# Kernel optimization log

Measured on AMD Instinct MI355X. Metric: run time of the kernel, lower is better.

## Reference

```python
import jax, jax.numpy as jnp
import numpy as np

B, L, D, H, V = 4, 128, 128, 8, 32000
N_ITER = 4
DAMP_H = DAMP_Z = DAMP_X = 0.0
STEP_H = STEP_Z = STEP_X = 1.0
REG_H = REG_Z = REG_X = 1.0
BLOCK_MSG = False
NEG = 1e9


def _norm(t):
    # norm='softmax'
    return jax.nn.softmax(t, axis=-1)


def setup_inputs() -> dict:
    key = jax.random.key(0)
    k1, k2, k3, k4 = jax.random.split(key, 4)
    x = jax.random.normal(k1, (B, L, D), dtype=jnp.float32)
    mask = jnp.ones((B, L), dtype=jnp.int32)
    m_mask = jax.random.randint(k2, (B, L), 0, 2).astype(jnp.int32)
    embed_matrix = jax.random.normal(k3, (V, D), dtype=jnp.float32)
    ternary = jax.random.normal(k4, (2, D, D, H), dtype=jnp.float32)  # dists='' -> 2 groups
    return {"x": x, "mask": mask, "embed_matrix": embed_matrix, "m_mask": m_mask, "ternary": ternary}


def _forward(x, mask, embed_matrix, m_mask, ternary):
    dt = x.dtype
    mask1d = mask != 0                                   # [B,L] True = real token
    valid2d = mask1d[:, :, None] & mask1d[:, None, :]    # [B,L,L]
    inv2d = ~valid2d[:, None, :, :]                      # broadcast over heads
    keep = mask1d[..., None].astype(dt)                  # [B,L,1]
    mm = m_mask.astype(dt)[..., None]                    # [B,L,1]

    # distance mask: dists='' -> [triu(1); tril(-1)] -> [2,L,L]
    dm = jnp.triu(jnp.ones((L, L), dt), 1)
    distmask = jnp.stack([dm, dm.T], axis=0)

    eye = jnp.eye(L, dtype=dt)

    unary = x
    q_x = jnp.ones((B, L, V), dt)
    # initialize_Z=True: masked positions start from expected embedding
    pre = _norm(q_x) @ embed_matrix                      # [B,L,D]
    q_z = unary * (1.0 - mm) + pre * mm
    q_z = q_z * keep

    q_h = jnp.ones((B, H, L, L), dt) - eye * NEG
    q_h = jnp.where(inv2d, -NEG, q_h)

    cache_qh, cache_qz, cache_qx = q_h, q_z, q_x
    # async_update=True: normalize Z before first H update
    q_z = _norm(q_z) * keep

    for _ in range(N_ITER):
        # ---- H update: F[z,c,i,j] = sum_{k,a,b} q_z[z,i,a] q_z[z,j,b] T[k,a,b,c] dist[k,i,j]
        t1 = jnp.einsum('zia,kabc->zkibc', q_z, ternary)            # [B,2,L,D,H]
        F = jnp.einsum('zkibc,zjb,kij->zcij', t1, q_z, distmask)    # [B,H,L,L]
        q_h = cache_qh * DAMP_H + F * (1.0 - DAMP_H) / REG_H
        q_h = cache_qh * (1.0 - STEP_H) + q_h * STEP_H
        cache_qh = q_h
        q_h = q_h - eye * NEG
        q_h = jnp.where(inv2d, -NEG, q_h)
        q_hn = _norm(q_h)                                           # [B,H,L,L]

        # ---- Z update: first-order messages from ternary factors
        m = q_hn[:, None] * distmask[None, :, None]                 # [B,2,H,L,L]
        s1 = jnp.einsum('zkcij,zjb->zkibc', m, q_z)                 # to Z_i (head slot)
        G = jnp.einsum('zkibc,kabc->zia', s1, ternary)
        if not BLOCK_MSG:
            s2 = jnp.einsum('zkcij,zia->zkjac', m, q_z)             # to Z_j (dep slot)
            G = G + jnp.einsum('zkjac,kabc->zjb', s2, ternary)

        # unary: X message replaces word unary at <MASK> positions
        unary_eff = unary * (1.0 - mm) + (_norm(q_x) @ embed_matrix) * mm
        q_z_new = cache_qz * DAMP_Z + (unary_eff + G) * (1.0 - DAMP_Z) / REG_Z
        q_z_new = cache_qz * (1.0 - STEP_Z) + q_z_new * STEP_Z
        cache_qz = q_z_new
        q_z = _norm(q_z_new) * keep

        # ---- X update: message from Z through embedding factor
        msg_x = jnp.einsum('zia,va->ziv', q_z, embed_matrix)        # [B,L,V]
        q_x_new = cache_qx * DAMP_X + msg_x * (1.0 - DAMP_X) / REG_X
        q_x_new = cache_qx * (1.0 - STEP_X) + q_x_new * STEP_X
        cache_qx = q_x_new
        q_x = q_x_new

    # output_prob=False -> unnormalized scores
    return q_x


def reference(x, mask, embed_matrix, m_mask, ternary):
    return _forward(x, mask, embed_matrix, m_mask, ternary)
```

## Files before the change

kernel.cpp:

```cpp
#include <hip/hip_runtime.h>
#include <math.h>

#define L_ 128
#define D_ 128
#define H_ 8
#define V_ 32000
#define NEGC 1e9f

typedef short short8 __attribute__((ext_vector_type(8)));
typedef float f32x4 __attribute__((ext_vector_type(4)));
typedef unsigned short ushort8v __attribute__((ext_vector_type(8)));

__device__ __forceinline__ unsigned short f2bf(float x) {
    unsigned int u = __float_as_uint(x);
    unsigned int r = (u + 0x7fff + ((u >> 16) & 1)) >> 16;
    return (unsigned short)r;
}


__global__ __launch_bounds__(256) void colsum_k(const float* __restrict__ E, float* __restrict__ meansum) {
    int t = threadIdx.x;
    int d = t & 127, h = t >> 7;
    int v0 = blockIdx.x * 256;
    float s = 0.f;
    for (int p = 0; p < 128; ++p)
        s += E[(v0 + h + 2 * p) * 128 + d];
    __shared__ float red[256];
    red[t] = s;
    __syncthreads();
    if (h == 0) atomicAdd(&meansum[d], red[d] + red[128 + d]);
}

__global__ __launch_bounds__(256) void frag_k(const float* __restrict__ E,
                                              unsigned short* __restrict__ Ebf,
                                              unsigned short* __restrict__ Etf) {
    __shared__ unsigned short tile[32][136];
    int t = threadIdx.x;
    int b = blockIdx.x;
    int v0 = b * 32;
#pragma unroll
    for (int i = 0; i < 4; ++i) {
        int idx = i * 256 + t;
        int v = idx >> 5;
        int d4 = (idx & 31) * 4;
        float4 val = *(const float4*)&E[(size_t)(v0 + v) * 128 + d4];
        tile[v][d4 + 0] = f2bf(val.x);
        tile[v][d4 + 1] = f2bf(val.y);
        tile[v][d4 + 2] = f2bf(val.z);
        tile[v][d4 + 3] = f2bf(val.w);
    }
    __syncthreads();
    {
        int fi = t >> 5;
        int l0 = (t & 31) * 2;
        int vtl = fi >> 2, s = fi & 3;
        size_t base = ((size_t)(b * 2 + vtl) * 4 + s) * 512;
#pragma unroll
        for (int li = 0; li < 2; ++li) {
            int l = l0 + li;
            int nl = l & 15, hf = l >> 4;
            ushort8v o;
#pragma unroll
            for (int j = 0; j < 8; ++j) o[j] = tile[vtl * 16 + nl][s * 32 + hf * 8 + j];
            *(ushort8v*)&Ebf[base + l * 8] = o;
        }
    }
    {
        int ct = t >> 5;
        int l0 = (t & 31) * 2;
        size_t base = ((size_t)b * 8 + ct) * 512;
#pragma unroll
        for (int li = 0; li < 2; ++li) {
            int l = l0 + li;
            int nl = l & 15, hf = l >> 4;
            ushort8v o;
#pragma unroll
            for (int j = 0; j < 8; ++j) o[j] = tile[hf * 8 + j][ct * 16 + nl];
            *(ushort8v*)&Etf[base + l * 8] = o;
        }
    }
}

__global__ __launch_bounds__(256) void transT_k(const float* __restrict__ T, float* __restrict__ Tt) {
    for (int q = 0; q < 4; ++q) {
        int id = blockIdx.x * 1024 + q * 256 + threadIdx.x;
        int k = id >> 17;
        int rem = id & 131071;
        int a = rem >> 10;
        int bc = rem & 1023;
        int b = bc >> 3, c = bc & 7;
        Tt[k * 131072 + b * 1024 + a * 8 + c] = T[id];
    }
}

__global__ __launch_bounds__(512) void compact_k(const int* __restrict__ m_mask,
                                                 int* __restrict__ rowidx, int* __restrict__ nactb) {
    int t = threadIdx.x;
    bool act = m_mask[t] != 0;
    unsigned long long b = __ballot(act);
    int w = t >> 6, lane = t & 63;
    __shared__ int wc[8];
    if (lane == 0) wc[w] = __popcll(b);
    __syncthreads();
    int base = 0;
    for (int i = 0; i < w; ++i) base += wc[i];
    if (act) rowidx[base + __popcll(b & ((1ull << lane) - 1))] = t;
    if (t == 0) {
        int tot = 0;
        for (int i = 0; i < 8; ++i) tot += wc[i];
        nactb[0] = tot;
    }
}

__global__ __launch_bounds__(64) void init_k(const float* __restrict__ x, const int* __restrict__ mask,
                                             const int* __restrict__ m_mask, const float* __restrict__ meansum,
                                             float* __restrict__ ue, float* __restrict__ qz,
                                             unsigned short* __restrict__ qzb) {
    int row = blockIdx.x, t = threadIdx.x;
    float keepv = mask[row] ? 1.f : 0.f;
    bool mm = m_mask[row] != 0;
    float pre0 = meansum[t] * (1.f / 32000.f);
    float pre1 = meansum[t + 64] * (1.f / 32000.f);
    float u0 = mm ? pre0 : x[row * 128 + t];
    float u1 = mm ? pre1 : x[row * 128 + t + 64];
    ue[row * 128 + t] = u0;
    ue[row * 128 + t + 64] = u1;
    float sv0 = u0 * keepv, sv1 = u1 * keepv;
    float m = fmaxf(sv0, sv1);
    for (int off = 32; off; off >>= 1) m = fmaxf(m, __shfl_xor(m, off));
    float e0 = __expf(sv0 - m), e1 = __expf(sv1 - m);
    float s = e0 + e1;
    for (int off = 32; off; off >>= 1) s += __shfl_xor(s, off);
    float inv = keepv / s;
    float q0 = e0 * inv, q1 = e1 * inv;
    qz[row * 128 + t] = q0;
    qz[row * 128 + t + 64] = q1;
    qzb[row * 128 + t] = f2bf(q0);
    qzb[row * 128 + t + 64] = f2bf(q1);
}


__global__ __launch_bounds__(256) void pxe_k(const unsigned short* __restrict__ qzb,
                                             const unsigned short* __restrict__ Ebf,
                                             const unsigned short* __restrict__ Etf,
                                             const int* __restrict__ rowidx, const int* __restrict__ nactb,
                                             float* __restrict__ partial, float* __restrict__ partial_rs) {
    int nact = nactb[0];
    int bid = blockIdx.x;
    int xcd = bid & 7, idx = bid >> 3;
    int g = xcd + 8 * (idx >> 5);
    int bx = idx & 31;
    int r0 = bx * 16;
    if (g >= 50 || r0 >= nact) return;
    int t = threadIdx.x;
    int w = t >> 6, lane = t & 63;
    int nloc = lane & 15, half = lane >> 4;
    __shared__ __align__(16) unsigned short Pl[4][2][16 * 36];
    __shared__ float slab[4][16 * 130];
    __shared__ float rsW[4][16];
    int rA = r0 + nloc;
    bool actA = rA < nact;
    int rowA = actA ? rowidx[rA] : 0;
    short8 zero8 = (short8){0, 0, 0, 0, 0, 0, 0, 0};
    short8 afr[4];
#pragma unroll
    for (int s = 0; s < 4; ++s) {
        short8 v = *(const short8*)&qzb[rowA * 128 + s * 32 + half * 8];
        afr[s] = actA ? v : zero8;
    }
    const int kc0 = g * 20 + w * 5;
    short8 ebb[2][8];
#pragma unroll
    for (int f = 0; f < 8; ++f)
        ebb[0][f] = *(const short8*)&Ebf[((size_t)(kc0 * 8 + f)) * 512 + lane * 8];
    f32x4 acc2[8];
#pragma unroll
    for (int ct = 0; ct < 8; ++ct) acc2[ct] = (f32x4){0.f, 0.f, 0.f, 0.f};
    float rsl = 0.f;
#pragma unroll
    for (int step = 0; step < 5; ++step) {
        const int p = step & 1;
        const int kc = kc0 + step;
        short8 et[8];
#pragma unroll
        for (int f = 0; f < 8; ++f)
            et[f] = *(const short8*)&Etf[((size_t)(kc * 8 + f)) * 512 + lane * 8];
        if (step < 4) {
#pragma unroll
            for (int f = 0; f < 8; ++f)
                ebb[p ^ 1][f] = *(const short8*)&Ebf[((size_t)((kc + 1) * 8 + f)) * 512 + lane * 8];
        }
        f32x4 p0 = (f32x4){0.f, 0.f, 0.f, 0.f};
        f32x4 p1 = (f32x4){0.f, 0.f, 0.f, 0.f};
#pragma unroll
        for (int s = 0; s < 4; ++s) {
            p0 = __builtin_amdgcn_mfma_f32_16x16x32_bf16(ebb[p][s], afr[s], p0, 0, 0, 0);
            p1 = __builtin_amdgcn_mfma_f32_16x16x32_bf16(ebb[p][4 + s], afr[s], p1, 0, 0, 0);
        }
        unsigned short* pw = &Pl[w][p][0];
        {
            float e0 = __expf(p0[0]), e1 = __expf(p0[1]), e2 = __expf(p0[2]), e3 = __expf(p0[3]);
            rsl += (e0 + e1) + (e2 + e3);
            uint2 pk = {(unsigned)f2bf(e0) | ((unsigned)f2bf(e1) << 16),
                        (unsigned)f2bf(e2) | ((unsigned)f2bf(e3) << 16)};
            *(uint2*)&pw[nloc * 36 + half * 4] = pk;
        }
        {
            float e0 = __expf(p1[0]), e1 = __expf(p1[1]), e2 = __expf(p1[2]), e3 = __expf(p1[3]);
            rsl += (e0 + e1) + (e2 + e3);
            uint2 pk = {(unsigned)f2bf(e0) | ((unsigned)f2bf(e1) << 16),
                        (unsigned)f2bf(e2) | ((unsigned)f2bf(e3) << 16)};
            *(uint2*)&pw[nloc * 36 + 16 + half * 4] = pk;
        }
        short8 a2 = *(const short8*)&pw[nloc * 36 + half * 8];
#pragma unroll
        for (int ct = 0; ct < 8; ++ct)
            acc2[ct] = __builtin_amdgcn_mfma_f32_16x16x32_bf16(a2, et[ct], acc2[ct], 0, 0, 0);
    }
    rsl += __shfl_xor(rsl, 16);
    rsl += __shfl_xor(rsl, 32);
    if (lane < 16) rsW[w][nloc] = rsl;
#pragma unroll
    for (int ct = 0; ct < 8; ++ct)
#pragma unroll
        for (int reg = 0; reg < 4; ++reg)
            slab[w][(half * 4 + reg) * 130 + ct * 16 + nloc] = acc2[ct][reg];
    __syncthreads();
    float* pb = partial + (size_t)g * 65536;
    for (int i = t; i < 2048; i += 256) {
        int row = i >> 7, col = i & 127;
        int rr = r0 + row;
        if (rr < nact)
            pb[rr * 128 + col] = slab[0][row * 130 + col] + slab[1][row * 130 + col]
                               + slab[2][row * 130 + col] + slab[3][row * 130 + col];
    }
    if (t < 16) {
        int rr = r0 + t;
        if (rr < nact)
            partial_rs[g * 512 + rr] = rsW[0][t] + rsW[1][t] + rsW[2][t] + rsW[3][t];
    }
}

__global__ __launch_bounds__(256) void reduce_k(const float* __restrict__ partial,
                                                const float* __restrict__ partial_rs,
                                                const int* __restrict__ rowidx, const int* __restrict__ nactb,
                                                float* __restrict__ exbuf, float* __restrict__ rowsum) {
    int nact = nactb[0];
    int idx = blockIdx.x * 256 + threadIdx.x;
    int rr = idx >> 7, col = idx & 127;
    if (rr >= nact) return;
    float s = 0.f;
#pragma unroll 10
    for (int g = 0; g < 50; ++g)
        s += partial[(size_t)g * 65536 + rr * 128 + col];
    int row = rowidx[rr];
    exbuf[row * 128 + col] = s;
    if (col == 0) {
        float ts = 0.f;
#pragma unroll 10
        for (int g = 0; g < 50; ++g) ts += partial_rs[g * 512 + rr];
        rowsum[row] = ts;
    }
}

__global__ __launch_bounds__(256) void uwgemm_k(const float* __restrict__ qz, const float* __restrict__ T,
                                                const float* __restrict__ Tt, float* __restrict__ U2,
                                                unsigned short* __restrict__ Ut, unsigned short* __restrict__ Wt) {
    int t = threadIdx.x;
    int by = blockIdx.y;
    int uw = by >> 3, z = (by >> 1) & 3, k = by & 1;
    int bx = blockIdx.x;
    int m0 = (bx >> 2) * 16, n = (bx & 3) * 256 + t;
    const float* A = qz + z * 16384;
    const float* Bm = (uw ? Tt : T) + k * 131072;
    __shared__ float aL[2048];
    for (int idx = t; idx < 2048; idx += 256)
        aL[idx] = A[(m0 + (idx >> 7)) * 128 + (idx & 127)];
    __syncthreads();
    float acc[16];
#pragma unroll
    for (int m = 0; m < 16; ++m) acc[m] = 0.f;
    for (int kq = 0; kq < 32; ++kq) {
        float b0 = Bm[(kq * 4 + 0) * 1024 + n];
        float b1 = Bm[(kq * 4 + 1) * 1024 + n];
        float b2 = Bm[(kq * 4 + 2) * 1024 + n];
        float b3 = Bm[(kq * 4 + 3) * 1024 + n];
#pragma unroll
        for (int m = 0; m < 16; ++m) {
            const float4 aq = *(const float4*)&aL[m * 128 + kq * 4];
            acc[m] += aq.x * b0 + aq.y * b1 + aq.z * b2 + aq.w * b3;
        }
    }
    if (uw == 0) {
        float* Cm = U2 + (z * 2 + k) * 131072;
#pragma unroll
        for (int m = 0; m < 16; ++m)
            Cm[(m0 + m) * 1024 + n] = acc[m];
    }
    int bb = n >> 3, cc = n & 7;
    ushort8v p0, p1;
#pragma unroll
    for (int m = 0; m < 8; ++m) { p0[m] = f2bf(acc[m]); p1[m] = f2bf(acc[8 + m]); }
    unsigned short* To = (uw ? Wt : Ut) + ((size_t)(z * 2 + k) * 128 + bb) * 1024 + cc * 128 + m0;
    *(ushort8v*)&To[0] = p0;
    *(ushort8v*)&To[8] = p1;
}

__global__ __launch_bounds__(256) void qhnF_k(const float* __restrict__ qz, const float* __restrict__ U2,
                                              const int* __restrict__ mask,
                                              unsigned short* __restrict__ A0b, unsigned short* __restrict__ A1b,
                                              unsigned short* __restrict__ A0Tb, unsigned short* __restrict__ A1Tb) {
    int bx = blockIdx.x;
    int z = bx >> 6, c = (bx >> 3) & 7, iq = bx & 7;
    int i0 = iq * 16;
    int t = threadIdx.x;
    int tj = t & 15, ti = t >> 4;
    int i = i0 + ti;
    __shared__ float As[2][16][36];
    __shared__ float Bs[128][36];
    __shared__ int maskL[128];
    if (t < 128) maskL[t] = mask[z * 128 + t];
    float acc0[8], acc1[8];
#pragma unroll
    for (int jj = 0; jj < 8; ++jj) { acc0[jj] = 0.f; acc1[jj] = 0.f; }
    const float* U2z = U2 + (size_t)z * 262144;
    const float* qzz = qz + z * 16384;
    for (int kb = 0; kb < 4; ++kb) {
        int b0 = kb * 32;
        __syncthreads();
        for (int e = t; e < 1024; e += 256) {
            int k = e >> 9, r = e & 511, ii = r >> 5, b = r & 31;
            As[k][ii][b] = U2z[k * 131072 + (i0 + ii) * 1024 + (b0 + b) * 8 + c];
        }
        for (int f = t; f < 1024; f += 256) {
            int j = f >> 3, b4 = f & 7;
            int slot = b4 ^ ((j >> 3) & 7);
            *(float4*)&Bs[j][slot * 4] = *(const float4*)&qzz[j * 128 + b0 + b4 * 4];
        }
        __syncthreads();
#pragma unroll
        for (int b4 = 0; b4 < 8; ++b4) {
            float4 a0 = *(const float4*)&As[0][ti][b4 * 4];
            float4 a1 = *(const float4*)&As[1][ti][b4 * 4];
#pragma unroll
            for (int jj = 0; jj < 8; ++jj) {
                int j = tj * 8 + jj;
                int slot = b4 ^ ((j >> 3) & 7);
                float4 bq = *(const float4*)&Bs[j][slot * 4];
                acc0[jj] += a0.x * bq.x;
                acc0[jj] += a0.y * bq.y;
                acc0[jj] += a0.z * bq.z;
                acc0[jj] += a0.w * bq.w;
                acc1[jj] += a1.x * bq.x;
                acc1[jj] += a1.y * bq.y;
                acc1[jj] += a1.z * bq.z;
                acc1[jj] += a1.w * bq.w;
            }
        }
    }
    bool vi = maskL[i] != 0;
    float fv[8];
#pragma unroll
    for (int jj = 0; jj < 8; ++jj) {
        int j2 = tj * 8 + jj;
        float F = (j2 > i) ? acc0[jj] : acc1[jj];
        if (j2 == i) F -= NEGC;
        if (!vi || maskL[j2] == 0) F = -NEGC;
        fv[jj] = F;
    }
    float mval = fv[0];
#pragma unroll
    for (int jj = 1; jj < 8; ++jj) mval = fmaxf(mval, fv[jj]);
    for (int off = 1; off < 16; off <<= 1) mval = fmaxf(mval, __shfl_xor(mval, off));
    float ssum = 0.f;
#pragma unroll
    for (int jj = 0; jj < 8; ++jj) ssum += __expf(fv[jj] - mval);
    for (int off = 1; off < 16; off <<= 1) ssum += __shfl_xor(ssum, off);
    float inv = 1.f / ssum;
    size_t base = (size_t)(z * 8 + c) * 16384;
    ushort8v v0, v1;
    unsigned short bvv[8];
#pragma unroll
    for (int jj = 0; jj < 8; ++jj) {
        int j2 = tj * 8 + jj;
        float val = __expf(fv[jj] - mval) * inv;
        unsigned short bv = f2bf(val);
        bvv[jj] = bv;
        v0[jj] = (j2 > i) ? bv : (unsigned short)0;
        v1[jj] = (j2 < i) ? bv : (unsigned short)0;
    }
    *(ushort8v*)&A0b[base + i * 128 + tj * 8] = v0;
    *(ushort8v*)&A1b[base + i * 128 + tj * 8] = v1;
#pragma unroll
    for (int jj = 0; jj < 8; ++jj) {
        int j2 = tj * 8 + jj;
        A0Tb[base + j2 * 128 + i] = (i < j2) ? bvv[jj] : (unsigned short)0;
        A1Tb[base + j2 * 128 + i] = (i > j2) ? bvv[jj] : (unsigned short)0;
    }
}

__global__ __launch_bounds__(64) void gkern_mfma_k(const unsigned short* __restrict__ A0b,
                                                   const unsigned short* __restrict__ A1b,
                                                   const unsigned short* __restrict__ A0Tb,
                                                   const unsigned short* __restrict__ A1Tb,
                                                   const unsigned short* __restrict__ Ut,
                                                   const unsigned short* __restrict__ Wt,
                                                   float* __restrict__ g1, float* __restrict__ g2) {
    int mode = blockIdx.y;
    int bx = blockIdx.x;
    int z = bx >> 6, it = (bx >> 3) & 7, at = bx & 7;
    int lane = threadIdx.x;
    int nloc = lane & 15, half = lane >> 4;
    int i0 = it * 16, a0 = at * 16;
    const unsigned short* Am0 = (mode ? A0Tb : A0b) + (size_t)z * 131072;
    const unsigned short* Am1 = (mode ? A1Tb : A1b) + (size_t)z * 131072;
    const unsigned short* Bt = mode ? Ut : Wt;
    const unsigned short* B0 = Bt + (size_t)(z * 2 + 0) * 131072 + (size_t)(a0 + nloc) * 1024;
    const unsigned short* B1 = Bt + (size_t)(z * 2 + 1) * 131072 + (size_t)(a0 + nloc) * 1024;
    const unsigned short* Ar0 = Am0 + (size_t)(i0 + nloc) * 128;
    const unsigned short* Ar1 = Am1 + (size_t)(i0 + nloc) * 128;
    f32x4 acc = (f32x4){0.f, 0.f, 0.f, 0.f};
#pragma unroll
    for (int c = 0; c < 8; ++c) {
#pragma unroll
        for (int sb = 0; sb < 4; ++sb) {
            int s0 = sb * 32 + half * 8;
            short8 av0 = *(const short8*)&Ar0[c * 16384 + s0];
            short8 bv0 = *(const short8*)&B0[c * 128 + s0];
            acc = __builtin_amdgcn_mfma_f32_16x16x32_bf16(av0, bv0, acc, 0, 0, 0);
            short8 av1 = *(const short8*)&Ar1[c * 16384 + s0];
            short8 bv1 = *(const short8*)&B1[c * 128 + s0];
            acc = __builtin_amdgcn_mfma_f32_16x16x32_bf16(av1, bv1, acc, 0, 0, 0);
        }
    }
    float* G = mode ? g2 : g1;
#pragma unroll
    for (int reg = 0; reg < 4; ++reg)
        G[(z * 128 + i0 + half * 4 + reg) * 128 + a0 + nloc] = acc[reg];
}

__global__ __launch_bounds__(64) void zupd_k(const float* __restrict__ ue, const float* __restrict__ x,
                                             const int* __restrict__ m_mask,
                                             const float* __restrict__ exbuf, const float* __restrict__ rowsum,
                                             const float* __restrict__ g1, const float* __restrict__ g2,
                                             const int* __restrict__ mask,
                                             float* __restrict__ qz, unsigned short* __restrict__ qzb, int useEx) {
    int row = blockIdx.x, t = threadIdx.x;
    float keepv = mask[row] ? 1.f : 0.f;
    int b = row * 128;
    float u0, u1;
    if (useEx) {
        if (m_mask[row] != 0) {
            float rsv = rowsum[row];
            u0 = exbuf[b + t] / rsv;
            u1 = exbuf[b + t + 64] / rsv;
        } else {
            u0 = x[b + t];
            u1 = x[b + t + 64];
        }
    } else {
        u0 = ue[b + t];
        u1 = ue[b + t + 64];
    }
    float v0 = u0 + g1[b + t] + g2[b + t];
    float v1 = u1 + g1[b + t + 64] + g2[b + t + 64];
    float m = fmaxf(v0, v1);
    for (int off = 32; off; off >>= 1) m = fmaxf(m, __shfl_xor(m, off));
    float e0 = __expf(v0 - m), e1 = __expf(v1 - m);
    float s = e0 + e1;
    for (int off = 32; off; off >>= 1) s += __shfl_xor(s, off);
    float inv = keepv / s;
    float q0 = e0 * inv, q1 = e1 * inv;
    qz[b + t] = q0;
    qz[b + t + 64] = q1;
    qzb[b + t] = f2bf(q0);
    qzb[b + t + 64] = f2bf(q1);
}

__global__ __launch_bounds__(256) void msgx_mfma_k(const unsigned short* __restrict__ qzb,
                                                   const unsigned short* __restrict__ Ebf,
                                                   float* __restrict__ out) {
    int t = threadIdx.x;
    int w = t >> 6, lane = t & 63;
    int nloc = lane & 15, half = lane >> 4;
    int rt0 = blockIdx.x * 64;
    int cb0 = blockIdx.y * 256 + w * 64;
    short8 afr[4][4];
#pragma unroll
    for (int r = 0; r < 4; ++r)
#pragma unroll
        for (int s = 0; s < 4; ++s)
            afr[r][s] = *(const short8*)&qzb[(rt0 + r * 16 + nloc) * 128 + s * 32 + half * 8];
    f32x4 acc[4][4];
#pragma unroll
    for (int r = 0; r < 4; ++r)
#pragma unroll
        for (int ct = 0; ct < 4; ++ct)
            acc[r][ct] = (f32x4){0.f, 0.f, 0.f, 0.f};
#pragma unroll
    for (int ct = 0; ct < 4; ++ct) {
#pragma unroll
        for (int s = 0; s < 4; ++s) {
            short8 bfr = *(const short8*)&Ebf[(((size_t)(cb0 >> 4) + ct) * 4 + s) * 512 + lane * 8];
#pragma unroll
            for (int r = 0; r < 4; ++r)
                acc[r][ct] = __builtin_amdgcn_mfma_f32_16x16x32_bf16(afr[r][s], bfr, acc[r][ct], 0, 0, 0);
        }
    }
#pragma unroll
    for (int r = 0; r < 4; ++r)
#pragma unroll
        for (int ct = 0; ct < 4; ++ct) {
            int col = cb0 + ct * 16 + nloc;
#pragma unroll
            for (int reg = 0; reg < 4; ++reg) {
                int row = rt0 + r * 16 + half * 4 + reg;
                out[(size_t)row * V_ + col] = acc[r][ct][reg];
            }
        }
}

extern "C" void kernel_launch(void* const* d_in, const int* in_sizes, int n_in,
                              void* d_out, int out_size, void* d_ws, size_t ws_size,
                              hipStream_t stream) {
    const float* x     = (const float*)d_in[0];
    const int*   mask  = (const int*)d_in[1];
    const float* E     = (const float*)d_in[2];
    const int*   mmask = (const int*)d_in[3];
    const float* T     = (const float*)d_in[4];
    float* out = (float*)d_out;

    float* w = (float*)d_ws;
    float* meansum = w;
    float* ue      = w + 128;
    float* qz      = ue + 65536;
    float* exbuf   = qz + 65536;
    float* rowsum  = exbuf + 65536;
    float* g1      = rowsum + 512;
    float* g2      = g1 + 65536;
    float* Tt      = g2 + 65536;
    float* U2      = Tt + 262144;
    float* prs     = U2 + 1048576;
    unsigned short* qzb  = (unsigned short*)(prs + 25600);
    unsigned short* Ebf  = qzb + 65536;
    unsigned short* Etf  = Ebf + 4096000;
    unsigned short* A0b  = Etf + 4096000;
    unsigned short* A1b  = A0b + 524288;
    unsigned short* A0Tb = A1b + 524288;
    unsigned short* A1Tb = A0Tb + 524288;
    unsigned short* Ut   = A1Tb + 524288;
    unsigned short* Wt   = Ut + 1048576;
    int* rowidx = (int*)(Wt + 1048576);
    int* nactb  = rowidx + 512;

    float* partial = out;

    hipMemsetAsync(meansum, 0, 128 * sizeof(float), stream);
    colsum_k<<<125, 256, 0, stream>>>(E, meansum);
    frag_k<<<1000, 256, 0, stream>>>(E, Ebf, Etf);
    transT_k<<<256, 256, 0, stream>>>(T, Tt);
    compact_k<<<1, 512, 0, stream>>>(mmask, rowidx, nactb);
    init_k<<<512, 64, 0, stream>>>(x, mask, mmask, meansum, ue, qz, qzb);

    for (int it = 0; it < 4; ++it) {
        if (it) {
            pxe_k<<<1792, 256, 0, stream>>>(qzb, Ebf, Etf, rowidx, nactb, partial, prs);
            reduce_k<<<256, 256, 0, stream>>>(partial, prs, rowidx, nactb, exbuf, rowsum);
        }
        uwgemm_k<<<dim3(32, 16), 256, 0, stream>>>(qz, T, Tt, U2, Ut, Wt);
        qhnF_k<<<256, 256, 0, stream>>>(qz, U2, mask, A0b, A1b, A0Tb, A1Tb);
        gkern_mfma_k<<<dim3(256, 2), 64, 0, stream>>>(A0b, A1b, A0Tb, A1Tb, Ut, Wt, g1, g2);
        zupd_k<<<512, 64, 0, stream>>>(ue, x, mmask, exbuf, rowsum, g1, g2, mask, qz, qzb, it ? 1 : 0);
    }
    msgx_mfma_k<<<dim3(8, 125), 256, 0, stream>>>(qzb, Ebf, out);
}
```

Baseline: 412.2 us.

## Merge independent kernels into multi-role launches to cut launch count

Folds the three setup kernels (bf16 fragment packing, ternary transpose, mask compaction) into one launch that picks its role from the block index. In each iteration the independent U/W GEMM and the expectation GEMM (pxe) now share one launch, as do the partial reduction and the qh/F kernel. This removes about eight launch gaps per forward and lets independent work overlap on the device. The cost is a larger shared-memory footprint per block, sized for the biggest role, which may lower occupancy for the smaller roles.

After: 381.4 us. 7.5% less time.

```diff
diff --git a/kernel.cpp b/kernel.cpp
--- a/kernel.cpp
+++ b/kernel.cpp
@@ -31,84 +31,90 @@
     if (h == 0) atomicAdd(&meansum[d], red[d] + red[128 + d]);
 }
 
-__global__ __launch_bounds__(256) void frag_k(const float* __restrict__ E,
+__global__ __launch_bounds__(256) void prep_k(const float* __restrict__ E,
                                               unsigned short* __restrict__ Ebf,
-                                              unsigned short* __restrict__ Etf) {
-    __shared__ unsigned short tile[32][136];
+                                              unsigned short* __restrict__ Etf,
+                                              const float* __restrict__ T, float* __restrict__ Tt,
+                                              const int* __restrict__ m_mask,
+                                              int* __restrict__ rowidx, int* __restrict__ nactb) {
+    __shared__ __align__(16) unsigned char psmem[8704];
+    int blk = blockIdx.x;
     int t = threadIdx.x;
-    int b = blockIdx.x;
-    int v0 = b * 32;
-#pragma unroll
-    for (int i = 0; i < 4; ++i) {
-        int idx = i * 256 + t;
-        int v = idx >> 5;
-        int d4 = (idx & 31) * 4;
-        float4 val = *(const float4*)&E[(size_t)(v0 + v) * 128 + d4];
-        tile[v][d4 + 0] = f2bf(val.x);
-        tile[v][d4 + 1] = f2bf(val.y);
-        tile[v][d4 + 2] = f2bf(val.z);
-        tile[v][d4 + 3] = f2bf(val.w);
-    }
-    __syncthreads();
-    {
-        int fi = t >> 5;
-        int l0 = (t & 31) * 2;
-        int vtl = fi >> 2, s = fi & 3;
-        size_t base = ((size_t)(b * 2 + vtl) * 4 + s) * 512;
-#pragma unroll
-        for (int li = 0; li < 2; ++li) {
-            int l = l0 + li;
-            int nl = l & 15, hf = l >> 4;
-            ushort8v o;
-#pragma unroll
-            for (int j = 0; j < 8; ++j) o[j] = tile[vtl * 16 + nl][s * 32 + hf * 8 + j];
-            *(ushort8v*)&Ebf[base + l * 8] = o;
-        }
-    }
-    {
-        int ct = t >> 5;
-        int l0 = (t & 31) * 2;
-        size_t base = ((size_t)b * 8 + ct) * 512;
-#pragma unroll
-        for (int li = 0; li < 2; ++li) {
-            int l = l0 + li;
-            int nl = l & 15, hf = l >> 4;
-            ushort8v o;
-#pragma unroll
-            for (int j = 0; j < 8; ++j) o[j] = tile[hf * 8 + j][ct * 16 + nl];
-            *(ushort8v*)&Etf[base + l * 8] = o;
-        }
-    }
-}
-
-__global__ __launch_bounds__(256) void transT_k(const float* __restrict__ T, float* __restrict__ Tt) {
-    for (int q = 0; q < 4; ++q) {
-        int id = blockIdx.x * 1024 + q * 256 + threadIdx.x;
-        int k = id >> 17;
-        int rem = id & 131071;
-        int a = rem >> 10;
-        int bc = rem & 1023;
-        int b = bc >> 3, c = bc & 7;
-        Tt[k * 131072 + b * 1024 + a * 8 + c] = T[id];
-    }
-}
-
-__global__ __launch_bounds__(512) void compact_k(const int* __restrict__ m_mask,
-                                                 int* __restrict__ rowidx, int* __restrict__ nactb) {
-    int t = threadIdx.x;
-    bool act = m_mask[t] != 0;
-    unsigned long long b = __ballot(act);
-    int w = t >> 6, lane = t & 63;
-    __shared__ int wc[8];
-    if (lane == 0) wc[w] = __popcll(b);
-    __syncthreads();
-    int base = 0;
-    for (int i = 0; i < w; ++i) base += wc[i];
-    if (act) rowidx[base + __popcll(b & ((1ull << lane) - 1))] = t;
-    if (t == 0) {
-        int tot = 0;
-        for (int i = 0; i < 8; ++i) tot += wc[i];
-        nactb[0] = tot;
+    if (blk < 1000) {
+        unsigned short* tile = (unsigned short*)psmem;
+        int v0 = blk * 32;
+#pragma unroll
+        for (int i = 0; i < 4; ++i) {
+            int idx = i * 256 + t;
+            int v = idx >> 5;
+            int d4 = (idx & 31) * 4;
+            float4 val = *(const float4*)&E[(size_t)(v0 + v) * 128 + d4];
+            tile[v * 136 + d4 + 0] = f2bf(val.x);
+            tile[v * 136 + d4 + 1] = f2bf(val.y);
+            tile[v * 136 + d4 + 2] = f2bf(val.z);
+            tile[v * 136 + d4 + 3] = f2bf(val.w);
+        }
+        __syncthreads();
+        {
+            int fi = t >> 5;
+            int l0 = (t & 31) * 2;
+            int vtl = fi >> 2, s = fi & 3;
+            size_t base = ((size_t)(blk * 2 + vtl) * 4 + s) * 512;
+#pragma unroll
+            for (int li = 0; li < 2; ++li) {
+                int l = l0 + li;
+                int nl = l & 15, hf = l >> 4;
+                ushort8v o;
+#pragma unroll
+                for (int j = 0; j < 8; ++j) o[j] = tile[(vtl * 16 + nl) * 136 + s * 32 + hf * 8 + j];
+                *(ushort8v*)&Ebf[base + l * 8] = o;
+            }
+        }
+        {
+            int ct = t >> 5;
+            int l0 = (t & 31) * 2;
+            size_t base = ((size_t)blk * 8 + ct) * 512;
+#pragma unroll
+            for (int li = 0; li < 2; ++li) {
+                int l = l0 + li;
+                int nl = l & 15, hf = l >> 4;
+                ushort8v o;
+#pragma unroll
+                for (int j = 0; j < 8; ++j) o[j] = tile[(hf * 8 + j) * 136 + ct * 16 + nl];
+                *(ushort8v*)&Etf[base + l * 8] = o;
+            }
+        }
+    } else if (blk < 1256) {
+        int tb = blk - 1000;
+        for (int q = 0; q < 4; ++q) {
+            int id = tb * 1024 + q * 256 + t;
+            int k = id >> 17;
+            int rem = id & 131071;
+            int a = rem >> 10;
+            int bc = rem & 1023;
+            int b = bc >> 3, c = bc & 7;
+            Tt[k * 131072 + b * 1024 + a * 8 + c] = T[id];
+        }
+    } else {
+        int* wc = (int*)psmem;
+        bool a0 = m_mask[t] != 0;
+        bool a1 = m_mask[t + 256] != 0;
+        unsigned long long b0 = __ballot(a0);
+        unsigned long long b1 = __ballot(a1);
+        int w = t >> 6, lane = t & 63;
+        if (lane == 0) { wc[w] = __popcll(b0); wc[4 + w] = __popcll(b1); }
+        __syncthreads();
+        int base0 = 0;
+        for (int i = 0; i < w; ++i) base0 += wc[i];
+        int base1 = 0;
+        for (int i = 0; i < 4 + w; ++i) base1 += wc[i];
+        if (a0) rowidx[base0 + __popcll(b0 & ((1ull << lane) - 1))] = t;
+        if (a1) rowidx[base1 + __popcll(b1 & ((1ull << lane) - 1))] = t + 256;
+        if (t == 0) {
+            int tot = 0;
+            for (int i = 0; i < 8; ++i) tot += wc[i];
+            nactb[0] = tot;
+        }
     }
 }
 
@@ -140,185 +146,188 @@
 }
 
 
-__global__ __launch_bounds__(256) void pxe_k(const unsigned short* __restrict__ qzb,
-                                             const unsigned short* __restrict__ Ebf,
-                                             const unsigned short* __restrict__ Etf,
-                                             const int* __restrict__ rowidx, const int* __restrict__ nactb,
-                                             float* __restrict__ partial, float* __restrict__ partial_rs) {
-    int nact = nactb[0];
-    int bid = blockIdx.x;
-    int xcd = bid & 7, idx = bid >> 3;
-    int g = xcd + 8 * (idx >> 5);
-    int bx = idx & 31;
-    int r0 = bx * 16;
-    if (g >= 50 || r0 >= nact) return;
+__global__ __launch_bounds__(256) void fusedA_k(const float* __restrict__ qz, const float* __restrict__ T,
+                                                const float* __restrict__ Tt, float* __restrict__ U2,
+                                                unsigned short* __restrict__ Ut, unsigned short* __restrict__ Wt,
+                                                const unsigned short* __restrict__ qzb,
+                                                const unsigned short* __restrict__ Ebf,
+                                                const unsigned short* __restrict__ Etf,
+                                                const int* __restrict__ rowidx, const int* __restrict__ nactb,
+                                                float* __restrict__ partial, float* __restrict__ partial_rs) {
+    __shared__ __align__(16) unsigned char smem[42752];
+    int blk = blockIdx.x;
     int t = threadIdx.x;
-    int w = t >> 6, lane = t & 63;
-    int nloc = lane & 15, half = lane >> 4;
-    __shared__ __align__(16) unsigned short Pl[4][2][16 * 36];
-    __shared__ float slab[4][16 * 130];
-    __shared__ float rsW[4][16];
-    int rA = r0 + nloc;
-    bool actA = rA < nact;
-    int rowA = actA ? rowidx[rA] : 0;
-    short8 zero8 = (short8){0, 0, 0, 0, 0, 0, 0, 0};
-    short8 afr[4];
-#pragma unroll
-    for (int s = 0; s < 4; ++s) {
-        short8 v = *(const short8*)&qzb[rowA * 128 + s * 32 + half * 8];
-        afr[s] = actA ? v : zero8;
-    }
-    const int kc0 = g * 20 + w * 5;
-    short8 ebb[2][8];
-#pragma unroll
-    for (int f = 0; f < 8; ++f)
-        ebb[0][f] = *(const short8*)&Ebf[((size_t)(kc0 * 8 + f)) * 512 + lane * 8];
-    f32x4 acc2[8];
-#pragma unroll
-    for (int ct = 0; ct < 8; ++ct) acc2[ct] = (f32x4){0.f, 0.f, 0.f, 0.f};
-    float rsl = 0.f;
-#pragma unroll
-    for (int step = 0; step < 5; ++step) {
-        const int p = step & 1;
-        const int kc = kc0 + step;
-        short8 et[8];
+    if (blk < 512) {
+        float* aL = (float*)smem;
+        int by = blk >> 5;
+        int uw = by >> 3, z = (by >> 1) & 3, k = by & 1;
+        int bx = blk & 31;
+        int m0 = (bx >> 2) * 16, n = (bx & 3) * 256 + t;
+        const float* A = qz + z * 16384;
+        const float* Bm = (uw ? Tt : T) + k * 131072;
+        for (int idx = t; idx < 2048; idx += 256)
+            aL[idx] = A[(m0 + (idx >> 7)) * 128 + (idx & 127)];
+        __syncthreads();
+        float acc[16];
+#pragma unroll
+        for (int m = 0; m < 16; ++m) acc[m] = 0.f;
+        for (int kq = 0; kq < 32; ++kq) {
+            float b0 = Bm[(kq * 4 + 0) * 1024 + n];
+            float b1 = Bm[(kq * 4 + 1) * 1024 + n];
+            float b2 = Bm[(kq * 4 + 2) * 1024 + n];
+            float b3 = Bm[(kq * 4 + 3) * 1024 + n];
+#pragma unroll
+            for (int m = 0; m < 16; ++m) {
+                const float4 aq = *(const float4*)&aL[m * 128 + kq * 4];
+                acc[m] += aq.x * b0 + aq.y * b1 + aq.z * b2 + aq.w * b3;
+            }
+        }
+        if (uw == 0) {
+            float* Cm = U2 + (z * 2 + k) * 131072;
+#pragma unroll
+            for (int m = 0; m < 16; ++m)
+                Cm[(m0 + m) * 1024 + n] = acc[m];
+        }
+        int bb = n >> 3, cc = n & 7;
+        ushort8v p0, p1;
+#pragma unroll
+        for (int m = 0; m < 8; ++m) { p0[m] = f2bf(acc[m]); p1[m] = f2bf(acc[8 + m]); }
+        unsigned short* To = (uw ? Wt : Ut) + ((size_t)(z * 2 + k) * 128 + bb) * 1024 + cc * 128 + m0;
+        *(ushort8v*)&To[0] = p0;
+        *(ushort8v*)&To[8] = p1;
+    } else {
+        int nact = nactb[0];
+        int bid = blk - 512;
+        int xcd = bid & 7, idx = bid >> 3;
+        int g = xcd + 8 * (idx >> 5);
+        int bx = idx & 31;
+        int r0 = bx * 16;
+        if (g >= 50 || r0 >= nact) return;
+        unsigned short* Pl = (unsigned short*)smem;
+        float* slab = (float*)(smem + 9216);
+        float* rsW  = (float*)(smem + 9216 + 33280);
+        int w = t >> 6, lane = t & 63;
+        int nloc = lane & 15, half = lane >> 4;
+        int rA = r0 + nloc;
+        bool actA = rA < nact;
+        int rowA = actA ? rowidx[rA] : 0;
+        short8 zero8 = (short8){0, 0, 0, 0, 0, 0, 0, 0};
+        short8 afr[4];
+#pragma unroll
+        for (int s = 0; s < 4; ++s) {
+            short8 v = *(const short8*)&qzb[rowA * 128 + s * 32 + half * 8];
+            afr[s] = actA ? v : zero8;
+        }
+        const int kc0 = g * 20 + w * 5;
+        short8 ebb[2][8];
 #pragma unroll
         for (int f = 0; f < 8; ++f)
-            et[f] = *(const short8*)&Etf[((size_t)(kc * 8 + f)) * 512 + lane * 8];
-        if (step < 4) {
+            ebb[0][f] = *(const short8*)&Ebf[((size_t)(kc0 * 8 + f)) * 512 + lane * 8];
+        f32x4 acc2[8];
+#pragma unroll
+        for (int ct = 0; ct < 8; ++ct) acc2[ct] = (f32x4){0.f, 0.f, 0.f, 0.f};
+        float rsl = 0.f;
+#pragma unroll
+        for (int step = 0; step < 5; ++step) {
+            const int p = step & 1;
+            const int kc = kc0 + step;
+            short8 et[8];
 #pragma unroll
             for (int f = 0; f < 8; ++f)
-                ebb[p ^ 1][f] = *(const short8*)&Ebf[((size_t)((kc + 1) * 8 + f)) * 512 + lane * 8];
-        }
-        f32x4 p0 = (f32x4){0.f, 0.f, 0.f, 0.f};
-        f32x4 p1 = (f32x4){0.f, 0.f, 0.f, 0.f};
-#pragma unroll
-        for (int s = 0; s < 4; ++s) {
-            p0 = __builtin_amdgcn_mfma_f32_16x16x32_bf16(ebb[p][s], afr[s], p0, 0, 0, 0);
-            p1 = __builtin_amdgcn_mfma_f32_16x16x32_bf16(ebb[p][4 + s], afr[s], p1, 0, 0, 0);
-        }
-        unsigned short* pw = &Pl[w][p][0];
-        {
-            float e0 = __expf(p0[0]), e1 = __expf(p0[1]), e2 = __expf(p0[2]), e3 = __expf(p0[3]);
-            rsl += (e0 + e1) + (e2 + e3);
-            uint2 pk = {(unsigned)f2bf(e0) | ((unsigned)f2bf(e1) << 16),
-                        (unsigned)f2bf(e2) | ((unsigned)f2bf(e3) << 16)};
-            *(uint2*)&pw[nloc * 36 + half * 4] = pk;
-        }
-        {
-            float e0 = __expf(p1[0]), e1 = __expf(p1[1]), e2 = __expf(p1[2]), e3 = __expf(p1[3]);
-            rsl += (e0 + e1) + (e2 + e3);
-            uint2 pk = {(unsigned)f2bf(e0) | ((unsigned)f2bf(e1) << 16),
-                        (unsigned)f2bf(e2) | ((unsigned)f2bf(e3) << 16)};
-            *(uint2*)&pw[nloc * 36 + 16 + half * 4] = pk;
-        }
-        short8 a2 = *(const short8*)&pw[nloc * 36 + half * 8];
+                et[f] = *(const short8*)&Etf[((size_t)(kc * 8 + f)) * 512 + lane * 8];
+            if (step < 4) {
+#pragma unroll
+                for (int f = 0; f < 8; ++f)
+                    ebb[p ^ 1][f] = *(const short8*)&Ebf[((size_t)((kc + 1) * 8 + f)) * 512 + lane * 8];
+            }
+            f32x4 p0 = (f32x4){0.f, 0.f, 0.f, 0.f};
+            f32x4 p1 = (f32x4){0.f, 0.f, 0.f, 0.f};
+#pragma unroll
+            for (int s = 0; s < 4; ++s) {
+                p0 = __builtin_amdgcn_mfma_f32_16x16x32_bf16(ebb[p][s], afr[s], p0, 0, 0, 0);
+                p1 = __builtin_amdgcn_mfma_f32_16x16x32_bf16(ebb[p][4 + s], afr[s], p1, 0, 0, 0);
+            }
+            unsigned short* pw = Pl + (w * 2 + p) * 576;
+            {
+                float e0 = __expf(p0[0]), e1 = __expf(p0[1]), e2 = __expf(p0[2]), e3 = __expf(p0[3]);
+                rsl += (e0 + e1) + (e2 + e3);
+                uint2 pk = {(unsigned)f2bf(e0) | ((unsigned)f2bf(e1) << 16),
+                            (unsigned)f2bf(e2) | ((unsigned)f2bf(e3) << 16)};
+                *(uint2*)&pw[nloc * 36 + half * 4] = pk;
+            }
+            {
+                float e0 = __expf(p1[0]), e1 = __expf(p1[1]), e2 = __expf(p1[2]), e3 = __expf(p1[3]);
+                rsl += (e0 + e1) + (e2 + e3);
+                uint2 pk = {(unsigned)f2bf(e0) | ((unsigned)f2bf(e1) << 16),
+                            (unsigned)f2bf(e2) | ((unsigned)f2bf(e3) << 16)};
+                *(uint2*)&pw[nloc * 36 + 16 + half * 4] = pk;
+            }
+            short8 a2 = *(const short8*)&pw[nloc * 36 + half * 8];
+#pragma unroll
+            for (int ct = 0; ct < 8; ++ct)
+                acc2[ct] = __builtin_amdgcn_mfma_f32_16x16x32_bf16(a2, et[ct], acc2[ct], 0, 0, 0);
+        }
+        rsl += __shfl_xor(rsl, 16);
+        rsl += __shfl_xor(rsl, 32);
+        if (lane < 16) rsW[w * 16 + nloc] = rsl;
 #pragma unroll
         for (int ct = 0; ct < 8; ++ct)
-            acc2[ct] = __builtin_amdgcn_mfma_f32_16x16x32_bf16(a2, et[ct], acc2[ct], 0, 0, 0);
-    }
-    rsl += __shfl_xor(rsl, 16);
-    rsl += __shfl_xor(rsl, 32);
-    if (lane < 16) rsW[w][nloc] = rsl;
-#pragma unroll
-    for (int ct = 0; ct < 8; ++ct)
-#pragma unroll
-        for (int reg = 0; reg < 4; ++reg)
-            slab[w][(half * 4 + reg) * 130 + ct * 16 + nloc] = acc2[ct][reg];
-    __syncthreads();
-    float* pb = partial + (size_t)g * 65536;
-    for (int i = t; i < 2048; i += 256) {
-        int row = i >> 7, col = i & 127;
-        int rr = r0 + row;
-        if (rr < nact)
-            pb[rr * 128 + col] = slab[0][row * 130 + col] + slab[1][row * 130 + col]
-                               + slab[2][row * 130 + col] + slab[3][row * 130 + col];
-    }
-    if (t < 16) {
-        int rr = r0 + t;
-        if (rr < nact)
-            partial_rs[g * 512 + rr] = rsW[0][t] + rsW[1][t] + rsW[2][t] + rsW[3][t];
-    }
-}
-
-__global__ __launch_bounds__(256) void reduce_k(const float* __restrict__ partial,
-                                                const float* __restrict__ partial_rs,
+#pragma unroll
+            for (int reg = 0; reg < 4; ++reg)
+                slab[w * 2080 + (half * 4 + reg) * 130 + ct * 16 + nloc] = acc2[ct][reg];
+        __syncthreads();
+        float* pb = partial + (size_t)g * 65536;
+        for (int i = t; i < 2048; i += 256) {
+            int row = i >> 7, col = i & 127;
+            int rr = r0 + row;
+            if (rr < nact)
+                pb[rr * 128 + col] = slab[row * 130 + col] + slab[2080 + row * 130 + col]
+                                   + slab[4160 + row * 130 + col] + slab[6240 + row * 130 + col];
+        }
+        if (t < 16) {
+            int rr = r0 + t;
+            if (rr < nact)
+                partial_rs[g * 512 + rr] = rsW[t] + rsW[16 + t] + rsW[32 + t] + rsW[48 + t];
+        }
+    }
+}
+
+__global__ __launch_bounds__(256) void fusedB_k(const float* __restrict__ qz, const float* __restrict__ U2,
+                                                const int* __restrict__ mask,
+                                                unsigned short* __restrict__ A0b, unsigned short* __restrict__ A1b,
+                                                unsigned short* __restrict__ A0Tb, unsigned short* __restrict__ A1Tb,
+                                                const float* __restrict__ partial, const float* __restrict__ partial_rs,
                                                 const int* __restrict__ rowidx, const int* __restrict__ nactb,
                                                 float* __restrict__ exbuf, float* __restrict__ rowsum) {
-    int nact = nactb[0];
-    int idx = blockIdx.x * 256 + threadIdx.x;
-    int rr = idx >> 7, col = idx & 127;
-    if (rr >= nact) return;
-    float s = 0.f;
+    __shared__ __align__(16) unsigned char smem[23552];
+    int blk = blockIdx.x;
+    int t = threadIdx.x;
+    if (blk >= 256) {
+        int nact = nactb[0];
+        int idx = (blk - 256) * 256 + t;
+        int rr = idx >> 7, col = idx & 127;
+        if (rr >= nact) return;
+        float s = 0.f;
 #pragma unroll 10
-    for (int g = 0; g < 50; ++g)
-        s += partial[(size_t)g * 65536 + rr * 128 + col];
-    int row = rowidx[rr];
-    exbuf[row * 128 + col] = s;
-    if (col == 0) {
-        float ts = 0.f;
+        for (int g = 0; g < 50; ++g)
+            s += partial[(size_t)g * 65536 + rr * 128 + col];
+        int row = rowidx[rr];
+        exbuf[row * 128 + col] = s;
+        if (col == 0) {
+            float ts = 0.f;
 #pragma unroll 10
-        for (int g = 0; g < 50; ++g) ts += partial_rs[g * 512 + rr];
-        rowsum[row] = ts;
-    }
-}
-
-__global__ __launch_bounds__(256) void uwgemm_k(const float* __restrict__ qz, const float* __restrict__ T,
-                                                const float* __restrict__ Tt, float* __restrict__ U2,
-                                                unsigned short* __restrict__ Ut, unsigned short* __restrict__ Wt) {
-    int t = threadIdx.x;
-    int by = blockIdx.y;
-    int uw = by >> 3, z = (by >> 1) & 3, k = by & 1;
-    int bx = blockIdx.x;
-    int m0 = (bx >> 2) * 16, n = (bx & 3) * 256 + t;
-    const float* A = qz + z * 16384;
-    const float* Bm = (uw ? Tt : T) + k * 131072;
-    __shared__ float aL[2048];
-    for (int idx = t; idx < 2048; idx += 256)
-        aL[idx] = A[(m0 + (idx >> 7)) * 128 + (idx & 127)];
-    __syncthreads();
-    float acc[16];
-#pragma unroll
-    for (int m = 0; m < 16; ++m) acc[m] = 0.f;
-    for (int kq = 0; kq < 32; ++kq) {
-        float b0 = Bm[(kq * 4 + 0) * 1024 + n];
-        float b1 = Bm[(kq * 4 + 1) * 1024 + n];
-        float b2 = Bm[(kq * 4 + 2) * 1024 + n];
-        float b3 = Bm[(kq * 4 + 3) * 1024 + n];
-#pragma unroll
-        for (int m = 0; m < 16; ++m) {
-            const float4 aq = *(const float4*)&aL[m * 128 + kq * 4];
-            acc[m] += aq.x * b0 + aq.y * b1 + aq.z * b2 + aq.w * b3;
-        }
-    }
-    if (uw == 0) {
-        float* Cm = U2 + (z * 2 + k) * 131072;
-#pragma unroll
-        for (int m = 0; m < 16; ++m)
-            Cm[(m0 + m) * 1024 + n] = acc[m];
-    }
-    int bb = n >> 3, cc = n & 7;
-    ushort8v p0, p1;
-#pragma unroll
-    for (int m = 0; m < 8; ++m) { p0[m] = f2bf(acc[m]); p1[m] = f2bf(acc[8 + m]); }
-    unsigned short* To = (uw ? Wt : Ut) + ((size_t)(z * 2 + k) * 128 + bb) * 1024 + cc * 128 + m0;
-    *(ushort8v*)&To[0] = p0;
-    *(ushort8v*)&To[8] = p1;
-}
-
-__global__ __launch_bounds__(256) void qhnF_k(const float* __restrict__ qz, const float* __restrict__ U2,
-                                              const int* __restrict__ mask,
-                                              unsigned short* __restrict__ A0b, unsigned short* __restrict__ A1b,
-                                              unsigned short* __restrict__ A0Tb, unsigned short* __restrict__ A1Tb) {
-    int bx = blockIdx.x;
-    int z = bx >> 6, c = (bx >> 3) & 7, iq = bx & 7;
+            for (int g = 0; g < 50; ++g) ts += partial_rs[g * 512 + rr];
+            rowsum[row] = ts;
+        }
+        return;
+    }
+    float* As = (float*)smem;
+    float* Bs = (float*)(smem + 4608);
+    int* maskL = (int*)(smem + 4608 + 18432);
+    int z = blk >> 6, c = (blk >> 3) & 7, iq = blk & 7;
     int i0 = iq * 16;
-    int t = threadIdx.x;
     int tj = t & 15, ti = t >> 4;
     int i = i0 + ti;
-    __shared__ float As[2][16][36];
-    __shared__ float Bs[128][36];
-    __shared__ int maskL[128];
     if (t < 128) maskL[t] = mask[z * 128 + t];
     float acc0[8], acc1[8];
 #pragma unroll
@@ -330,23 +339,23 @@
         __syncthreads();
         for (int e = t; e < 1024; e += 256) {
             int k = e >> 9, r = e & 511, ii = r >> 5, b = r & 31;
-            As[k][ii][b] = U2z[k * 131072 + (i0 + ii) * 1024 + (b0 + b) * 8 + c];
+            As[(k * 16 + ii) * 36 + b] = U2z[k * 131072 + (i0 + ii) * 1024 + (b0 + b) * 8 + c];
         }
         for (int f = t; f < 1024; f += 256) {
             int j = f >> 3, b4 = f & 7;
             int slot = b4 ^ ((j >> 3) & 7);
-            *(float4*)&Bs[j][slot * 4] = *(const float4*)&qzz[j * 128 + b0 + b4 * 4];
+            *(float4*)&Bs[j * 36 + slot * 4] = *(const float4*)&qzz[j * 128 + b0 + b4 * 4];
         }
         __syncthreads();
 #pragma unroll
         for (int b4 = 0; b4 < 8; ++b4) {
-            float4 a0 = *(const float4*)&As[0][ti][b4 * 4];
-            float4 a1 = *(const float4*)&As[1][ti][b4 * 4];
+            float4 a0 = *(const float4*)&As[(0 * 16 + ti) * 36 + b4 * 4];
+            float4 a1 = *(const float4*)&As[(1 * 16 + ti) * 36 + b4 * 4];
 #pragma unroll
             for (int jj = 0; jj < 8; ++jj) {
                 int j = tj * 8 + jj;
                 int slot = b4 ^ ((j >> 3) & 7);
-                float4 bq = *(const float4*)&Bs[j][slot * 4];
+                float4 bq = *(const float4*)&Bs[j * 36 + slot * 4];
                 acc0[jj] += a0.x * bq.x;
                 acc0[jj] += a0.y * bq.y;
                 acc0[jj] += a0.z * bq.z;
@@ -557,18 +566,14 @@
 
     hipMemsetAsync(meansum, 0, 128 * sizeof(float), stream);
     colsum_k<<<125, 256, 0, stream>>>(E, meansum);
-    frag_k<<<1000, 256, 0, stream>>>(E, Ebf, Etf);
-    transT_k<<<256, 256, 0, stream>>>(T, Tt);
-    compact_k<<<1, 512, 0, stream>>>(mmask, rowidx, nactb);
+    prep_k<<<1257, 256, 0, stream>>>(E, Ebf, Etf, T, Tt, mmask, rowidx, nactb);
     init_k<<<512, 64, 0, stream>>>(x, mask, mmask, meansum, ue, qz, qzb);
 
     for (int it = 0; it < 4; ++it) {
-        if (it) {
-            pxe_k<<<1792, 256, 0, stream>>>(qzb, Ebf, Etf, rowidx, nactb, partial, prs);
-            reduce_k<<<256, 256, 0, stream>>>(partial, prs, rowidx, nactb, exbuf, rowsum);
-        }
-        uwgemm_k<<<dim3(32, 16), 256, 0, stream>>>(qz, T, Tt, U2, Ut, Wt);
-        qhnF_k<<<256, 256, 0, stream>>>(qz, U2, mask, A0b, A1b, A0Tb, A1Tb);
+        fusedA_k<<<it ? 2304 : 512, 256, 0, stream>>>(qz, T, Tt, U2, Ut, Wt,
+                                                      qzb, Ebf, Etf, rowidx, nactb, partial, prs);
+        fusedB_k<<<it ? 512 : 256, 256, 0, stream>>>(qz, U2, mask, A0b, A1b, A0Tb, A1Tb,
+                                                     partial, prs, rowidx, nactb, exbuf, rowsum);
         gkern_mfma_k<<<dim3(256, 2), 64, 0, stream>>>(A0b, A1b, A0Tb, A1Tb, Ut, Wt, g1, g2);
         zupd_k<<<512, 64, 0, stream>>>(ue, x, mmask, exbuf, rowsum, g1, g2, mask, qz, qzb, it ? 1 : 0);
     }
```
